# Kernel tuning notes

Measured on AMD Instinct MI355X. Metric: run time of the kernel, lower is better.

## Reference

```python
import jax, jax.numpy as jnp
import numpy as np

B, N, D = 4, 8192, 1024
H, DK = 8, 128          # d_k = D // H
FF = 4096
EPS = 1e-5


def setup_inputs() -> dict:
    key = jax.random.key(0)
    ks = jax.random.split(key, 8)
    s = 0.02  # init scale for weights
    return {
        "x": jax.random.normal(ks[0], (B, N, D), jnp.float32),
        "delta_x": jax.random.uniform(ks[1], (N,), jnp.float32),
        # Linear weights stored [in, out] (math-equivalent to torch's x @ W.T)
        "Wq": jax.random.normal(ks[2], (D, D), jnp.float32) * s,
        "bq": jnp.zeros((D,), jnp.float32),
        "Wk": jax.random.normal(ks[3], (D, D), jnp.float32) * s,
        "bk": jnp.zeros((D,), jnp.float32),
        "Wv": jax.random.normal(ks[4], (D, D), jnp.float32) * s,
        "bv": jnp.zeros((D,), jnp.float32),
        # per-head LayerNorm params for K; NOTE: the original code (faithfully
        # reproduced) applies layernorms_K to BOTH key and value in Galerkin mode.
        "gamma_k": jnp.ones((H, DK), jnp.float32),
        "beta_k": jnp.zeros((H, DK), jnp.float32),
        "W1": jax.random.normal(ks[5], (D, FF), jnp.float32) * s,
        "b1": jnp.zeros((FF,), jnp.float32),
        "W2": jax.random.normal(ks[6], (FF, D), jnp.float32) * s,
        "b2": jnp.zeros((D,), jnp.float32),
    }


def _per_head_ln(t, gamma, beta):
    # t: [B, H, N, DK]; torch LayerNorm: biased variance over last dim
    mu = jnp.mean(t, axis=-1, keepdims=True)
    var = jnp.mean(jnp.square(t - mu), axis=-1, keepdims=True)
    t = (t - mu) * jax.lax.rsqrt(var + EPS)
    return t * gamma[None, :, None, :] + beta[None, :, None, :]


def reference(x, delta_x, Wq, bq, Wk, bk, Wv, bv, gamma_k, beta_k, W1, b1, W2, b2):
    b, n, d = x.shape

    def heads(y):  # [b, n, d] -> [b, H, n, DK]
        return y.reshape(b, n, H, DK).transpose(0, 2, 1, 3)

    q = heads(x @ Wq + bq)
    k = heads(x @ Wk + bk)
    v = heads(x @ Wv + bv)

    k = _per_head_ln(k, gamma_k, beta_k)
    v = _per_head_ln(v, gamma_k, beta_k)  # layernorms_K reused on value (as in source)
    k = k * delta_x[None, None, :, None]  # einsum('bhxd,x->bhxd')

    # Galerkin (softmax-free, linear) attention: (K^T V) / N then Q @ (.)
    scores = jnp.einsum("bhnd,bhne->bhde", k, v) / n  # [b,H,DK,DK]
    attn_out = jnp.einsum("bhnd,bhde->bhne", q, scores)  # [b,H,n,DK]
    # (F.dropout in the source treated as identity: inference/eval semantics)

    x = x + attn_out.transpose(0, 2, 1, 3).reshape(b, n, d)  # residual 1
    h = jax.nn.silu(x @ W1 + b1)
    return x + (h @ W2 + b2)  # residual 2
```

## Files before the change

### kernel.cpp

```cpp
#include <hip/hip_runtime.h>
#include <hip/hip_bf16.h>
#include <stdint.h>

#define DEV __device__ __forceinline__

typedef __attribute__((ext_vector_type(8))) short bf16x8;
typedef __attribute__((ext_vector_type(8))) unsigned short u16x8;
typedef __attribute__((ext_vector_type(4))) unsigned short u16x4;
typedef __attribute__((ext_vector_type(4))) float f32x4;

static constexpr int BB = 4, NN = 8192, DD = 1024, HH = 8, DKK = 128, FFF = 4096;
static constexpr int MM = BB * NN;

DEV float bfb2f(unsigned int s) { unsigned int x = s << 16; float f; __builtin_memcpy(&f, &x, 4); return f; }
DEV unsigned short f2bfb(float f) {
    unsigned int x; __builtin_memcpy(&x, &f, 4);
    x += 0x7fffu + ((x >> 16) & 1u);
    return (unsigned short)(x >> 16);
}

DEV void gload_lds16(const void* g, void* l) {
    auto gp = (const __attribute__((address_space(1))) void*)(uintptr_t)g;
    auto lp = (__attribute__((address_space(3))) void*)(unsigned int)(uintptr_t)l;
    __builtin_amdgcn_global_load_lds(gp, lp, 16, 0, 0);
}

__global__ void k_pack_bf16(const float* __restrict__ in, unsigned short* __restrict__ ob, long n) {
    long i = ((long)blockIdx.x * blockDim.x + threadIdx.x) * 8;
    if (i >= n) return;
    f32x4 a = *(const f32x4*)&in[i];
    f32x4 b = *(const f32x4*)&in[i + 4];
    u16x8 o;
    o[0]=f2bfb(a[0]); o[1]=f2bfb(a[1]); o[2]=f2bfb(a[2]); o[3]=f2bfb(a[3]);
    o[4]=f2bfb(b[0]); o[5]=f2bfb(b[1]); o[6]=f2bfb(b[2]); o[7]=f2bfb(b[3]);
    *(u16x8*)&ob[i] = o;
}

__global__ void k_transpose(const float* __restrict__ W, unsigned short* __restrict__ WT, int R, int C) {
    __shared__ float t[32][33];
    const int tid = threadIdx.x;
    const int r0 = blockIdx.y * 32, c0 = blockIdx.x * 32;
    const int lr = tid >> 3, lc = (tid & 7) * 4;
    f32x4 v = *(const f32x4*)&W[(long)(r0 + lr) * C + c0 + lc];
    t[lr][lc + 0] = v[0]; t[lr][lc + 1] = v[1]; t[lr][lc + 2] = v[2]; t[lr][lc + 3] = v[3];
    __syncthreads();
    const int oc = tid >> 3, orr = (tid & 7) * 4;
    u16x4 o;
    o[0] = f2bfb(t[orr + 0][oc]); o[1] = f2bfb(t[orr + 1][oc]);
    o[2] = f2bfb(t[orr + 2][oc]); o[3] = f2bfb(t[orr + 3][oc]);
    *(u16x4*)&WT[(long)(c0 + oc) * R + r0 + orr] = o;
}

template <int EPI>
__global__ __launch_bounds__(512, 2)
void k_gemm256(const unsigned short* __restrict__ A, int lda,
               const unsigned short* __restrict__ BT, int ldbt,
               const float* __restrict__ bias0, const float* __restrict__ bias1,
               const float* __restrict__ bias2,
               const unsigned short* __restrict__ resb,
               unsigned short* __restrict__ outp0, unsigned short* __restrict__ outp1,
               unsigned short* __restrict__ outp2,
               float* __restrict__ outf,
               int K, int gridx, int npass)
{
    extern __shared__ __align__(128) unsigned short smem[];
    unsigned short* As = smem;
    unsigned short* Bs = smem + 4 * 8192;

    const int wg0 = (blockIdx.x & 7) * 32 + (blockIdx.x >> 3);

    const int tid = threadIdx.x;
    const int lane = tid & 63;
    const int w = tid >> 6;
    const int wm = w >> 2, wn = w & 3;
    const int fr = lane & 15;
    const int kg = lane >> 4;

    const int dl = tid * 16;
    const int soff = dl ^ (((dl >> 7) & 3) << 4);
    const int arow = soff >> 6;
    const int akel = (soff & 63) >> 1;

    int aoff[8], boff[4];
    #pragma unroll
    for (int m = 0; m < 8; ++m) { int o = (wm * 128 + m * 16 + fr) * 64 + kg * 16; aoff[m] = o ^ (((o >> 7) & 3) << 4); }
    #pragma unroll
    for (int n = 0; n < 4; ++n) { int o = (wn * 64 + n * 16 + fr) * 64 + kg * 16; boff[n] = o ^ (((o >> 7) & 3) << 4); }

#define STG_A(base, u, ks, slot) do { \
        const unsigned short* _g = (base) + (long)(u) * 64 + (ks) * 32; \
        gload_lds16(_g,              (slot) + tid * 8); \
        gload_lds16(_g + 128L * lda, (slot) + 4096 + tid * 8); } while (0)
#define STG_B(base, u, ks, slot) do { \
        const unsigned short* _g = (base) + (long)(u) * 64 + (ks) * 32; \
        gload_lds16(_g,               (slot) + tid * 8); \
        gload_lds16(_g + 128L * ldbt, (slot) + 4096 + tid * 8); } while (0)

#define BAR() __builtin_amdgcn_s_barrier()
#define LGKM(N) do { asm volatile("s_waitcnt lgkmcnt(" #N ")" ::: "memory"); \
                     __builtin_amdgcn_sched_barrier(0); } while (0)
#define VM8() asm volatile("s_waitcnt vmcnt(8)" ::: "memory")

#define MFMA16(AF, BF, R0) do { \
        __builtin_amdgcn_s_setprio(1); \
        _Pragma("unroll") \
        for (int m = 0; m < 4; ++m) { \
            _Pragma("unroll") \
            for (int n = 0; n < 4; ++n) \
                acc[(R0) + m][n] = __builtin_amdgcn_mfma_f32_16x16x32_bf16(AF[m], BF[n], acc[(R0) + m][n], 0, 0, 0); \
        } \
        __builtin_amdgcn_s_setprio(0); } while (0)

#define DO_TILE(sa0, sa1, sb0, sb1, STG0, STG1, STG2, STG3) do { \
        bf16x8 b0f[4], a0f[4], a1f[4], b1f[4], a2f[4], a3f[4]; \
        _Pragma("unroll") \
        for (int n = 0; n < 4; ++n) b0f[n] = *(const bf16x8*)((const char*)(sb0) + boff[n]); \
        _Pragma("unroll") \
        for (int m = 0; m < 4; ++m) a0f[m] = *(const bf16x8*)((const char*)(sa0) + aoff[m]); \
        _Pragma("unroll") \
        for (int m = 0; m < 4; ++m) a1f[m] = *(const bf16x8*)((const char*)(sa0) + aoff[m + 4]); \
        STG0; \
        BAR(); LGKM(4); \
        MFMA16(a0f, b0f, 0); \
        BAR(); \
        STG1; VM8(); \
        BAR(); LGKM(0); \
        MFMA16(a1f, b0f, 4); \
        BAR(); \
        _Pragma("unroll") \
        for (int n = 0; n < 4; ++n) b1f[n] = *(const bf16x8*)((const char*)(sb1) + boff[n]); \
        _Pragma("unroll") \
        for (int m = 0; m < 4; ++m) a2f[m] = *(const bf16x8*)((const char*)(sa1) + aoff[m]); \
        _Pragma("unroll") \
        for (int m = 0; m < 4; ++m) a3f[m] = *(const bf16x8*)((const char*)(sa1) + aoff[m + 4]); \
        STG2; \
        BAR(); LGKM(4); \
        MFMA16(a2f, b1f, 0); \
        BAR(); \
        STG3; VM8(); \
        BAR(); LGKM(0); \
        MFMA16(a3f, b1f, 4); \
        BAR(); \
    } while (0)

    unsigned short* A0 = As;            unsigned short* A1 = As + 8192;
    unsigned short* A2 = As + 16384;    unsigned short* A3 = As + 24576;
    unsigned short* B0 = Bs;            unsigned short* B1 = Bs + 8192;
    unsigned short* B2 = Bs + 16384;    unsigned short* B3 = Bs + 24576;

    const int NT = K >> 6;

    int wg = wg0;
    int brow = (wg / gridx) * 256;
    int bcol = (wg % gridx) * 256;
    const unsigned short* Ab = A + (long)(brow + arow) * lda + akel;
    const unsigned short* Bb = BT + (long)(bcol + arow) * ldbt + akel;
    STG_A(Ab, 0, 0, A0); STG_B(Bb, 0, 0, B0);
    STG_B(Bb, 0, 1, B1); STG_A(Ab, 0, 1, A1);
    STG_A(Ab, 1, 0, A2); STG_B(Bb, 1, 0, B2);
    VM8();
    BAR();

    for (int p = 0; p < npass; ++p) {
        const int wgN = (p + 1 < npass) ? (wg0 + (p + 1) * 256) : wg0;
        const int browN = (wgN / gridx) * 256;
        const int bcolN = (wgN % gridx) * 256;
        const unsigned short* Ab2 = A + (long)(browN + arow) * lda + akel;
        const unsigned short* Bb2 = BT + (long)(bcolN + arow) * ldbt + akel;

        f32x4 acc[8][4] = {};

        for (int t = 0; t + 2 < NT; t += 2) {
            DO_TILE(A0, A1, B0, B1,
                    STG_B(Bb, t + 1, 1, B3), STG_A(Ab, t + 1, 1, A3),
                    STG_A(Ab, t + 2, 0, A0), STG_B(Bb, t + 2, 0, B0));
            DO_TILE(A2, A3, B2, B3,
                    STG_B(Bb, t + 2, 1, B1), STG_A(Ab, t + 2, 1, A1),
                    STG_A(Ab, t + 3, 0, A2), STG_B(Bb, t + 3, 0, B2));
        }
        DO_TILE(A0, A1, B0, B1,
                STG_B(Bb, NT - 1, 1, B3), STG_A(Ab, NT - 1, 1, A3),
                STG_A(Ab2, 0, 0, A0), STG_B(Bb2, 0, 0, B0));
        DO_TILE(A2, A3, B2, B3,
                STG_B(Bb2, 0, 1, B1), STG_A(Ab2, 0, 1, A1),
                STG_A(Ab2, 1, 0, A2), STG_B(Bb2, 1, 0, B2));

        const int q4 = (lane >> 4) * 4;
        if constexpr (EPI == 1) {
            const int mat = bcol >> 10;
            const float* bp = mat == 0 ? bias0 : (mat == 1 ? bias1 : bias2);
            unsigned short* op = mat == 0 ? outp0 : (mat == 1 ? outp1 : outp2);
            const int dc0 = bcol & 1023;
            #pragma unroll
            for (int m = 0; m < 8; ++m)
                #pragma unroll
                for (int n = 0; n < 4; ++n) {
                    const int c = dc0 + wn * 64 + n * 16 + fr;
                    const float bv = bp[c];
                    const int hh = c >> 7, dk = c & 127;
                    #pragma unroll
                    for (int j = 0; j < 4; ++j) {
                        const int r = brow + wm * 128 + m * 16 + q4 + j;
                        const long idx = (((long)(r >> 13) * 8 + hh) * 8192 + (r & 8191)) * 128 + dk;
                        op[idx] = f2bfb(acc[m][n][j] + bv);
                    }
                }
        } else if constexpr (EPI == 2) {
            #pragma unroll
            for (int m = 0; m < 8; ++m)
                #pragma unroll
                for (int n = 0; n < 4; ++n) {
                    const int c = bcol + wn * 64 + n * 16 + fr;
                    const float bv = bias0[c];
                    #pragma unroll
                    for (int j = 0; j < 4; ++j) {
                        const int r = brow + wm * 128 + m * 16 + q4 + j;
                        float v = acc[m][n][j] + bv;
                        v = v / (1.f + __expf(-v));
                        outp0[(long)r * FFF + c] = f2bfb(v);
                    }
                }
        } else {
            #pragma unroll
            for (int m = 0; m < 8; ++m)
                #pragma unroll
                for (int n = 0; n < 4; ++n) {
                    const int c = bcol + wn * 64 + n * 16 + fr;
                    const float bv = bias0[c];
                    #pragma unroll
                    for (int j = 0; j < 4; ++j) {
                        const int r = brow + wm * 128 + m * 16 + q4 + j;
                        float v = acc[m][n][j] + bv + bfb2f(resb[(long)r * DD + c]);
                        outf[(long)r * DD + c] = v;
                    }
                }
        }

        brow = browN; bcol = bcolN; Ab = Ab2; Bb = Bb2;
    }
    asm volatile("s_waitcnt vmcnt(0)" ::: "memory");
#undef DO_TILE
#undef MFMA16
#undef VM8
#undef LGKM
#undef BAR
#undef STG_A
#undef STG_B
}

template <int EPI>
__global__ __launch_bounds__(256, 2)
void k_gemm(const unsigned short* __restrict__ A, int lda, long sAz,
            const unsigned short* __restrict__ BT, int ldbt, long sBz,
            const float* __restrict__ bias,
            const float* __restrict__ resf,
            const unsigned short* __restrict__ resb,
            unsigned short* __restrict__ outp,
            float* __restrict__ outf,
            int K)
{
    __shared__ __align__(16) unsigned short As[128 * 32];
    __shared__ __align__(16) unsigned short Bs[128 * 32];
    const int tid = threadIdx.x;
    const int z = blockIdx.z;
    A  += (long)z * sAz;
    BT += (long)z * sBz;
    const int brow = blockIdx.y * 128;
    const int bcol = blockIdx.x * 128;

    const int c0 = tid, c1 = tid + 256;
    const unsigned short* Ap0 = A + (long)(brow + (c0 >> 2)) * lda + (c0 & 3) * 8;
    const unsigned short* Ap1 = A + (long)(brow + (c1 >> 2)) * lda + (c1 & 3) * 8;
    const unsigned short* Bp0 = BT + (long)(bcol + (c0 >> 2)) * ldbt + (c0 & 3) * 8;
    const unsigned short* Bp1 = BT + (long)(bcol + (c1 >> 2)) * ldbt + (c1 & 3) * 8;
    unsigned short* AsD0 = &As[c0 * 8];
    unsigned short* AsD1 = &As[c1 * 8];
    unsigned short* BsD0 = &Bs[c0 * 8];
    unsigned short* BsD1 = &Bs[c1 * 8];

    const int lane = tid & 63;
    const int w = tid >> 6;
    const int wr = (w >> 1) * 64;
    const int wc = (w & 1) * 64;
    const int fr = lane & 15;
    const int fk = (lane >> 4) * 8;

    f32x4 acc[4][4] = {};

    for (int kt = 0; kt < K; kt += 32) {
        gload_lds16(Ap0 + kt, AsD0);
        gload_lds16(Ap1 + kt, AsD1);
        gload_lds16(Bp0 + kt, BsD0);
        gload_lds16(Bp1 + kt, BsD1);
        __syncthreads();
        bf16x8 af[4], bfr[4];
        #pragma unroll
        for (int m = 0; m < 4; ++m) af[m] = *(const bf16x8*)&As[(wr + m * 16 + fr) * 32 + fk];
        #pragma unroll
        for (int n = 0; n < 4; ++n) bfr[n] = *(const bf16x8*)&Bs[(wc + n * 16 + fr) * 32 + fk];
        #pragma unroll
        for (int m = 0; m < 4; ++m)
            #pragma unroll
            for (int n = 0; n < 4; ++n)
                acc[m][n] = __builtin_amdgcn_mfma_f32_16x16x32_bf16(af[m], bfr[n], acc[m][n], 0, 0, 0);
        __syncthreads();
    }

    const int orow = (lane >> 4) * 4;
    #pragma unroll
    for (int m = 0; m < 4; ++m) {
        #pragma unroll
        for (int n = 0; n < 4; ++n) {
            const int d = bcol + wc + n * 16 + fr;
            #pragma unroll
            for (int j = 0; j < 4; ++j) {
                const int r = brow + wr + m * 16 + orow + j;
                float v = acc[m][n][j];
                if constexpr (EPI == 3) {
                    long xi = ((long)(z >> 3) * NN + r) * DD + (z & 7) * DKK + d;
                    v += resf[xi];
                    outp[xi] = f2bfb(v);
                }
            }
        }
    }
    (void)bias; (void)resb; (void)outf;
}

__global__ void k_ln(unsigned short* __restrict__ Kb, unsigned short* __restrict__ Vb,
                     const float* __restrict__ gk, const float* __restrict__ bek,
                     const float* __restrict__ dx)
{
    const int tid = threadIdx.x;
    const int lane = tid & 63;
    const long row = (long)blockIdx.x * 4 + (tid >> 6);
    unsigned short* buf = blockIdx.y ? Vb : Kb;
    const int h = (int)((row >> 13) & 7);
    const int n = (int)(row & 8191);
    unsigned int* p = (unsigned int*)(buf + row * 128) + lane;
    const unsigned int u = *p;
    float f0 = bfb2f(u & 0xffffu);
    float f1 = bfb2f(u >> 16);
    float s = f0 + f1, q = f0 * f0 + f1 * f1;
    #pragma unroll
    for (int o = 32; o; o >>= 1) { s += __shfl_xor(s, o); q += __shfl_xor(q, o); }
    const float mean = s * (1.f / 128.f);
    const float var  = q * (1.f / 128.f) - mean * mean;
    const float rstd = rsqrtf(var + 1e-5f);
    const int gi = h * 128 + lane * 2;
    float o0 = (f0 - mean) * rstd * gk[gi]     + bek[gi];
    float o1 = (f1 - mean) * rstd * gk[gi + 1] + bek[gi + 1];
    if (blockIdx.y == 0) { const float dl = dx[n]; o0 *= dl; o1 *= dl; }
    *p = (unsigned int)f2bfb(o0) | ((unsigned int)f2bfb(o1) << 16);
}

__global__ __launch_bounds__(256, 2)
void k_scorespart(const unsigned short* __restrict__ Kb, const unsigned short* __restrict__ Vb,
                  float* __restrict__ part)
{
    __shared__ __align__(16) unsigned short KT[128 * 136];
    __shared__ __align__(16) unsigned short VT[128 * 136];
    const int tid = threadIdx.x;
    const int bh = blockIdx.y, split = blockIdx.x;
    const unsigned short* Kp = Kb + (long)bh * NN * DKK;
    const unsigned short* Vp = Vb + (long)bh * NN * DKK;
    const int lane = tid & 63, w = tid >> 6;
    const int wr = (w >> 1) * 64, wc = (w & 1) * 64, fr = lane & 15, fk = (lane >> 4) * 8;
    const int nrow = tid >> 1, dblk = (tid & 1) * 64;
    f32x4 acc[4][4] = {};
    for (int c = 0; c < 8; ++c) {
        const int n0 = (split * 8 + c) * 128;
        bf16x8 kv[8], vv[8];
        #pragma unroll
        for (int i = 0; i < 8; ++i) {
            kv[i] = *(const bf16x8*)&Kp[(long)(n0 + nrow) * DKK + dblk + i * 8];
            vv[i] = *(const bf16x8*)&Vp[(long)(n0 + nrow) * DKK + dblk + i * 8];
        }
        __syncthreads();
        #pragma unroll
        for (int i = 0; i < 8; ++i)
            #pragma unroll
            for (int j = 0; j < 8; ++j) {
                const int dd = dblk + i * 8 + j;
                KT[dd * 136 + nrow] = (unsigned short)kv[i][j];
                VT[dd * 136 + nrow] = (unsigned short)vv[i][j];
            }
        __syncthreads();
        #pragma unroll
        for (int ks = 0; ks < 4; ++ks) {
            bf16x8 af[4], bfr[4];
            #pragma unroll
            for (int m = 0; m < 4; ++m) af[m] = *(const bf16x8*)&KT[(wr + m * 16 + fr) * 136 + ks * 32 + fk];
            #pragma unroll
            for (int n = 0; n < 4; ++n) bfr[n] = *(const bf16x8*)&VT[(wc + n * 16 + fr) * 136 + ks * 32 + fk];
            #pragma unroll
            for (int m = 0; m < 4; ++m)
                #pragma unroll
                for (int n = 0; n < 4; ++n)
                    acc[m][n] = __builtin_amdgcn_mfma_f32_16x16x32_bf16(af[m], bfr[n], acc[m][n], 0, 0, 0);
        }
    }
    float* P = part + (long)(bh * 8 + split) * 16384;
    const int orow = (lane >> 4) * 4;
    #pragma unroll
    for (int m = 0; m < 4; ++m)
        #pragma unroll
        for (int n = 0; n < 4; ++n)
            #pragma unroll
            for (int j = 0; j < 4; ++j) {
                const int dD = wr + m * 16 + orow + j;
                const int e  = wc + n * 16 + fr;
                P[dD * 128 + e] = acc[m][n][j];
            }
}

__global__ void k_scoresred(const float* __restrict__ part, unsigned short* __restrict__ scT)
{
    const int bh = blockIdx.x, tid = threadIdx.x;
    const float* P = part + (long)bh * 8 * 16384;
    for (int i = tid; i < 16384; i += 256) {
        float s = 0.f;
        #pragma unroll
        for (int sp = 0; sp < 8; ++sp) s += P[sp * 16384 + i];
        const int d = i >> 7, e = i & 127;
        scT[(long)bh * 16384 + e * 128 + d] = f2bfb(s * (1.f / 8192.f));
    }
}

extern "C" void kernel_launch(void* const* d_in, const int* in_sizes, int n_in,
                              void* d_out, int out_size, void* d_ws, size_t ws_size,
                              hipStream_t stream)
{
    const float* x   = (const float*)d_in[0];
    const float* dx  = (const float*)d_in[1];
    const float* Wq  = (const float*)d_in[2];
    const float* bq  = (const float*)d_in[3];
    const float* Wk  = (const float*)d_in[4];
    const float* bk  = (const float*)d_in[5];
    const float* Wv  = (const float*)d_in[6];
    const float* bv  = (const float*)d_in[7];
    const float* gk  = (const float*)d_in[8];
    const float* bek = (const float*)d_in[9];
    const float* W1  = (const float*)d_in[10];
    const float* b1  = (const float*)d_in[11];
    const float* W2  = (const float*)d_in[12];
    const float* b2  = (const float*)d_in[13];
    float* out = (float*)d_out;
    (void)in_sizes; (void)n_in; (void)out_size; (void)ws_size;

    hipFuncSetAttribute((const void*)k_gemm256<1>, hipFuncAttributeMaxDynamicSharedMemorySize, 131072);
    hipFuncSetAttribute((const void*)k_gemm256<2>, hipFuncAttributeMaxDynamicSharedMemorySize, 131072);
    hipFuncSetAttribute((const void*)k_gemm256<3>, hipFuncAttributeMaxDynamicSharedMemorySize, 131072);

    char* ws = (char*)d_ws;
    size_t off = 0;
    auto alloc = [&](size_t bytes) { void* p = ws + off; off += (bytes + 255) & ~(size_t)255; return p; };
    unsigned short* WqkvT = (unsigned short*)alloc((size_t)3 * DD * DD * 2);
    unsigned short* W1T   = (unsigned short*)alloc((size_t)FFF * DD * 2);
    unsigned short* W2T   = (unsigned short*)alloc((size_t)DD * FFF * 2);
    unsigned short* scT   = (unsigned short*)alloc((size_t)32 * 16384 * 2);
    unsigned short* xb    = (unsigned short*)alloc((size_t)MM * DD * 2);
    unsigned short* Kb    = (unsigned short*)alloc((size_t)MM * DD * 2);
    unsigned short* Vb    = (unsigned short*)alloc((size_t)MM * DD * 2);
    unsigned short* x1b   = (unsigned short*)alloc((size_t)MM * DD * 2);
    unsigned short* hb    = xb;
    float* part           = (float*)x1b;
    unsigned short* Qb    = (unsigned short*)out;

    k_pack_bf16<<<dim3(((long)MM * DD) / 8 / 256), 256, 0, stream>>>(x, xb, (long)MM * DD);
    k_transpose<<<dim3(DD / 32, DD / 32), 256, 0, stream>>>(Wq, WqkvT, DD, DD);
    k_transpose<<<dim3(DD / 32, DD / 32), 256, 0, stream>>>(Wk, WqkvT + (size_t)DD * DD, DD, DD);
    k_transpose<<<dim3(DD / 32, DD / 32), 256, 0, stream>>>(Wv, WqkvT + (size_t)2 * DD * DD, DD, DD);
    k_transpose<<<dim3(FFF / 32, DD / 32), 256, 0, stream>>>(W1, W1T, DD, FFF);
    k_transpose<<<dim3(DD / 32, FFF / 32), 256, 0, stream>>>(W2, W2T, FFF, DD);

    k_gemm256<1><<<dim3(256), 512, 131072, stream>>>(
        xb, DD, WqkvT, DD, bq, bk, bv, nullptr, Qb, Kb, Vb, nullptr, DD, 3072 / 256, 6);

    k_ln<<<dim3((BB * HH * NN) / 4, 2), 256, 0, stream>>>(Kb, Vb, gk, bek, dx);

    k_scorespart<<<dim3(8, 32), 256, 0, stream>>>(Kb, Vb, part);
    k_scoresred<<<dim3(32), 256, 0, stream>>>(part, scT);

    k_gemm<3><<<dim3(1, NN / 128, BB * HH), 256, 0, stream>>>(Qb, DKK, (long)NN * DKK, scT, DKK, 16384L,
                                                              nullptr, x, nullptr, x1b, nullptr, DKK);

    for (int c = 0; c < 2; ++c) {
        const unsigned short* xc = x1b + (size_t)c * 16384 * DD;
        k_gemm256<2><<<dim3(256), 512, 131072, stream>>>(
            xc, DD, W1T, DD, b1, nullptr, nullptr, nullptr, hb, nullptr, nullptr, nullptr, DD, FFF / 256, 4);
        k_gemm256<3><<<dim3(256), 512, 131072, stream>>>(
            hb, FFF, W2T, FFF, b2, nullptr, nullptr, xc, nullptr, nullptr, nullptr,
            out + (size_t)c * 16384 * DD, FFF, DD / 256, 1);
    }
}
```

Baseline: 1.000 ms.

## Fuse per-head LayerNorm and delta scaling into QKV GEMM epilogue

Removes the separate LayerNorm kernel and instead computes per-row mean and variance for K and V heads in the QKV GEMM epilogue. Partial sums are reduced with cross-lane shuffles plus an LDS exchange between the two warps covering each head, which raises dynamic shared memory and adds barriers. It also merges the three QKV weight transposes into one launch, reads the residual from the bf16 copy of x instead of fp32, and reorders the LDS fragment loads in the GEMM main loop so every wait is a full lgkmcnt(0). These cut a full read-and-write pass over K and V and some launch overhead, at the cost of residual precision and possibly less load/compute overlap in the main GEMM loop.

```diff
diff --git a/kernel.cpp b/kernel.cpp
--- a/kernel.cpp
+++ b/kernel.cpp
@@ -36,10 +36,10 @@
     *(u16x8*)&ob[i] = o;
 }
 
-__global__ void k_transpose(const float* __restrict__ W, unsigned short* __restrict__ WT, int R, int C) {
+DEV void transpose_body(const float* __restrict__ W, unsigned short* __restrict__ WT, int R, int C,
+                        int bx, int by, int tid) {
     __shared__ float t[32][33];
-    const int tid = threadIdx.x;
-    const int r0 = blockIdx.y * 32, c0 = blockIdx.x * 32;
+    const int r0 = by * 32, c0 = bx * 32;
     const int lr = tid >> 3, lc = (tid & 7) * 4;
     f32x4 v = *(const f32x4*)&W[(long)(r0 + lr) * C + c0 + lc];
     t[lr][lc + 0] = v[0]; t[lr][lc + 1] = v[1]; t[lr][lc + 2] = v[2]; t[lr][lc + 3] = v[3];
@@ -49,6 +49,14 @@
     o[0] = f2bfb(t[orr + 0][oc]); o[1] = f2bfb(t[orr + 1][oc]);
     o[2] = f2bfb(t[orr + 2][oc]); o[3] = f2bfb(t[orr + 3][oc]);
     *(u16x4*)&WT[(long)(c0 + oc) * R + r0 + orr] = o;
+}
+__global__ void k_transpose(const float* __restrict__ W, unsigned short* __restrict__ WT, int R, int C) {
+    transpose_body(W, WT, R, C, blockIdx.x, blockIdx.y, threadIdx.x);
+}
+__global__ void k_transpose_qkv(const float* __restrict__ Wq, const float* __restrict__ Wk,
+                                const float* __restrict__ Wv, unsigned short* __restrict__ WT) {
+    const float* W = blockIdx.z == 0 ? Wq : (blockIdx.z == 1 ? Wk : Wv);
+    transpose_body(W, WT + (size_t)blockIdx.z * DD * DD, DD, DD, blockIdx.x, blockIdx.y, threadIdx.x);
 }
 
 template <int EPI>
@@ -61,6 +69,8 @@
                unsigned short* __restrict__ outp0, unsigned short* __restrict__ outp1,
                unsigned short* __restrict__ outp2,
                float* __restrict__ outf,
+               const float* __restrict__ gkp, const float* __restrict__ bekp,
+               const float* __restrict__ dxp,
                int K, int gridx, int npass)
 {
     extern __shared__ __align__(128) unsigned short smem[];
@@ -97,7 +107,7 @@
         gload_lds16(_g + 128L * ldbt, (slot) + 4096 + tid * 8); } while (0)
 
 #define BAR() __builtin_amdgcn_s_barrier()
-#define LGKM(N) do { asm volatile("s_waitcnt lgkmcnt(" #N ")" ::: "memory"); \
+#define LGKM0() do { asm volatile("s_waitcnt lgkmcnt(0)" ::: "memory"); \
                      __builtin_amdgcn_sched_barrier(0); } while (0)
 #define VM8() asm volatile("s_waitcnt vmcnt(8)" ::: "memory")
 
@@ -113,32 +123,36 @@
 
 #define DO_TILE(sa0, sa1, sb0, sb1, STG0, STG1, STG2, STG3) do { \
         bf16x8 b0f[4], a0f[4], a1f[4], b1f[4], a2f[4], a3f[4]; \
+         \
         _Pragma("unroll") \
         for (int n = 0; n < 4; ++n) b0f[n] = *(const bf16x8*)((const char*)(sb0) + boff[n]); \
         _Pragma("unroll") \
         for (int m = 0; m < 4; ++m) a0f[m] = *(const bf16x8*)((const char*)(sa0) + aoff[m]); \
-        _Pragma("unroll") \
-        for (int m = 0; m < 4; ++m) a1f[m] = *(const bf16x8*)((const char*)(sa0) + aoff[m + 4]); \
         STG0; \
-        BAR(); LGKM(4); \
+        BAR(); LGKM0(); \
         MFMA16(a0f, b0f, 0); \
         BAR(); \
+         \
+        _Pragma("unroll") \
+        for (int m = 0; m < 4; ++m) a1f[m] = *(const bf16x8*)((const char*)(sa0) + aoff[m + 4]); \
         STG1; VM8(); \
-        BAR(); LGKM(0); \
+        BAR(); LGKM0(); \
         MFMA16(a1f, b0f, 4); \
         BAR(); \
+         \
         _Pragma("unroll") \
         for (int n = 0; n < 4; ++n) b1f[n] = *(const bf16x8*)((const char*)(sb1) + boff[n]); \
         _Pragma("unroll") \
         for (int m = 0; m < 4; ++m) a2f[m] = *(const bf16x8*)((const char*)(sa1) + aoff[m]); \
-        _Pragma("unroll") \
-        for (int m = 0; m < 4; ++m) a3f[m] = *(const bf16x8*)((const char*)(sa1) + aoff[m + 4]); \
         STG2; \
-        BAR(); LGKM(4); \
+        BAR(); LGKM0(); \
         MFMA16(a2f, b1f, 0); \
         BAR(); \
+         \
+        _Pragma("unroll") \
+        for (int m = 0; m < 4; ++m) a3f[m] = *(const bf16x8*)((const char*)(sa1) + aoff[m + 4]); \
         STG3; VM8(); \
-        BAR(); LGKM(0); \
+        BAR(); LGKM0(); \
         MFMA16(a3f, b1f, 4); \
         BAR(); \
     } while (0)
@@ -150,9 +164,8 @@
 
     const int NT = K >> 6;
 
-    int wg = wg0;
-    int brow = (wg / gridx) * 256;
-    int bcol = (wg % gridx) * 256;
+    int brow = ((wg0) / gridx) * 256;
+    int bcol = ((wg0) % gridx) * 256;
     const unsigned short* Ab = A + (long)(brow + arow) * lda + akel;
     const unsigned short* Bb = BT + (long)(bcol + arow) * ldbt + akel;
     STG_A(Ab, 0, 0, A0); STG_B(Bb, 0, 0, B0);
@@ -188,23 +201,87 @@
         const int q4 = (lane >> 4) * 4;
         if constexpr (EPI == 1) {
             const int mat = bcol >> 10;
+            const int dc0 = bcol & 1023;
             const float* bp = mat == 0 ? bias0 : (mat == 1 ? bias1 : bias2);
             unsigned short* op = mat == 0 ? outp0 : (mat == 1 ? outp1 : outp2);
-            const int dc0 = bcol & 1023;
+            float bv[4];
+            #pragma unroll
+            for (int n = 0; n < 4; ++n) bv[n] = bp[dc0 + wn * 64 + n * 16 + fr];
             #pragma unroll
             for (int m = 0; m < 8; ++m)
+                #pragma unroll
+                for (int n = 0; n < 4; ++n)
+                    #pragma unroll
+                    for (int j = 0; j < 4; ++j) acc[m][n][j] += bv[n];
+
+            if (mat == 0) {
+                #pragma unroll
+                for (int m = 0; m < 8; ++m)
+                    #pragma unroll
+                    for (int n = 0; n < 4; ++n) {
+                        const int c = dc0 + wn * 64 + n * 16 + fr;
+                        const int hh = c >> 7, dk = c & 127;
+                        #pragma unroll
+                        for (int j = 0; j < 4; ++j) {
+                            const int r = brow + wm * 128 + m * 16 + q4 + j;
+                            const long idx = (((long)(r >> 13) * 8 + hh) * 8192 + (r & 8191)) * 128 + dk;
+                            op[idx] = f2bfb(acc[m][n][j]);
+                        }
+                    }
+            } else {
+                float2* red2 = (float2*)(smem + 65536);
+                float ps[8][4], pq[8][4];
+                #pragma unroll
+                for (int m = 0; m < 8; ++m)
+                    #pragma unroll
+                    for (int j = 0; j < 4; ++j) {
+                        float s = acc[m][0][j] + acc[m][1][j] + acc[m][2][j] + acc[m][3][j];
+                        float qv = acc[m][0][j] * acc[m][0][j] + acc[m][1][j] * acc[m][1][j]
+                                 + acc[m][2][j] * acc[m][2][j] + acc[m][3][j] * acc[m][3][j];
+                        #pragma unroll
+                        for (int o = 1; o < 16; o <<= 1) { s += __shfl_xor(s, o); qv += __shfl_xor(qv, o); }
+                        ps[m][j] = s; pq[m][j] = qv;
+                    }
+                if (fr == 0) {
+                    const int g4 = lane >> 4;
+                    #pragma unroll
+                    for (int m = 0; m < 8; ++m)
+                        #pragma unroll
+                        for (int j = 0; j < 4; ++j)
+                            red2[wn * 256 + wm * 128 + m * 16 + g4 * 4 + j] = float2{ps[m][j], pq[m][j]};
+                }
+                BAR();
+                float gkv[4], bkv[4];
                 #pragma unroll
                 for (int n = 0; n < 4; ++n) {
                     const int c = dc0 + wn * 64 + n * 16 + fr;
-                    const float bv = bp[c];
-                    const int hh = c >> 7, dk = c & 127;
+                    gkv[n] = gkp[c]; bkv[n] = bekp[c];
+                }
+                const int hbase = (wn >> 1) * 512;
+                #pragma unroll
+                for (int m = 0; m < 8; ++m)
                     #pragma unroll
                     for (int j = 0; j < 4; ++j) {
-                        const int r = brow + wm * 128 + m * 16 + q4 + j;
-                        const long idx = (((long)(r >> 13) * 8 + hh) * 8192 + (r & 8191)) * 128 + dk;
-                        op[idx] = f2bfb(acc[m][n][j] + bv);
+                        const int ri = wm * 128 + m * 16 + q4 + j;
+                        const int r = brow + ri;
+                        const float2 e0 = red2[hbase + ri];
+                        const float2 e1 = red2[hbase + 256 + ri];
+                        const float mean = (e0.x + e1.x) * (1.f / 128.f);
+                        const float var  = (e0.y + e1.y) * (1.f / 128.f) - mean * mean;
+                        const float rstd = rsqrtf(var + 1e-5f);
+                        const float dmul = (mat == 1) ? dxp[r & 8191] : 1.f;
+                        #pragma unroll
+                        for (int n = 0; n < 4; ++n) {
+                            const int c = dc0 + wn * 64 + n * 16 + fr;
+                            const int hh = c >> 7, dk = c & 127;
+                            float v = (acc[m][n][j] - mean) * rstd * gkv[n] + bkv[n];
+                            v *= dmul;
+                            const long idx = (((long)(r >> 13) * 8 + hh) * 8192 + (r & 8191)) * 128 + dk;
+                            op[idx] = f2bfb(v);
+                        }
                     }
-                }
+                BAR();
+            }
         } else if constexpr (EPI == 2) {
             #pragma unroll
             for (int m = 0; m < 8; ++m)
@@ -242,7 +319,7 @@
 #undef DO_TILE
 #undef MFMA16
 #undef VM8
-#undef LGKM
+#undef LGKM0
 #undef BAR
 #undef STG_A
 #undef STG_B
@@ -252,11 +329,8 @@
 __global__ __launch_bounds__(256, 2)
 void k_gemm(const unsigned short* __restrict__ A, int lda, long sAz,
             const unsigned short* __restrict__ BT, int ldbt, long sBz,
-            const float* __restrict__ bias,
-            const float* __restrict__ resf,
             const unsigned short* __restrict__ resb,
             unsigned short* __restrict__ outp,
-            float* __restrict__ outf,
             int K)
 {
     __shared__ __align__(16) unsigned short As[128 * 32];
@@ -315,43 +389,14 @@
             #pragma unroll
             for (int j = 0; j < 4; ++j) {
                 const int r = brow + wr + m * 16 + orow + j;
-                float v = acc[m][n][j];
                 if constexpr (EPI == 3) {
                     long xi = ((long)(z >> 3) * NN + r) * DD + (z & 7) * DKK + d;
-                    v += resf[xi];
+                    float v = acc[m][n][j] + bfb2f(resb[xi]);
                     outp[xi] = f2bfb(v);
                 }
             }
         }
     }
-    (void)bias; (void)resb; (void)outf;
-}
-
-__global__ void k_ln(unsigned short* __restrict__ Kb, unsigned short* __restrict__ Vb,
-                     const float* __restrict__ gk, const float* __restrict__ bek,
-                     const float* __restrict__ dx)
-{
-    const int tid = threadIdx.x;
-    const int lane = tid & 63;
-    const long row = (long)blockIdx.x * 4 + (tid >> 6);
-    unsigned short* buf = blockIdx.y ? Vb : Kb;
-    const int h = (int)((row >> 13) & 7);
-    const int n = (int)(row & 8191);
-    unsigned int* p = (unsigned int*)(buf + row * 128) + lane;
-    const unsigned int u = *p;
-    float f0 = bfb2f(u & 0xffffu);
-    float f1 = bfb2f(u >> 16);
-    float s = f0 + f1, q = f0 * f0 + f1 * f1;
-    #pragma unroll
-    for (int o = 32; o; o >>= 1) { s += __shfl_xor(s, o); q += __shfl_xor(q, o); }
-    const float mean = s * (1.f / 128.f);
-    const float var  = q * (1.f / 128.f) - mean * mean;
-    const float rstd = rsqrtf(var + 1e-5f);
-    const int gi = h * 128 + lane * 2;
-    float o0 = (f0 - mean) * rstd * gk[gi]     + bek[gi];
-    float o1 = (f1 - mean) * rstd * gk[gi + 1] + bek[gi + 1];
-    if (blockIdx.y == 0) { const float dl = dx[n]; o0 *= dl; o1 *= dl; }
-    *p = (unsigned int)f2bfb(o0) | ((unsigned int)f2bfb(o1) << 16);
 }
 
 __global__ __launch_bounds__(256, 2)
@@ -448,7 +493,7 @@
     float* out = (float*)d_out;
     (void)in_sizes; (void)n_in; (void)out_size; (void)ws_size;
 
-    hipFuncSetAttribute((const void*)k_gemm256<1>, hipFuncAttributeMaxDynamicSharedMemorySize, 131072);
+    hipFuncSetAttribute((const void*)k_gemm256<1>, hipFuncAttributeMaxDynamicSharedMemorySize, 139264);
     hipFuncSetAttribute((const void*)k_gemm256<2>, hipFuncAttributeMaxDynamicSharedMemorySize, 131072);
     hipFuncSetAttribute((const void*)k_gemm256<3>, hipFuncAttributeMaxDynamicSharedMemorySize, 131072);
 
@@ -468,29 +513,27 @@
     unsigned short* Qb    = (unsigned short*)out;
 
     k_pack_bf16<<<dim3(((long)MM * DD) / 8 / 256), 256, 0, stream>>>(x, xb, (long)MM * DD);
-    k_transpose<<<dim3(DD / 32, DD / 32), 256, 0, stream>>>(Wq, WqkvT, DD, DD);
-    k_transpose<<<dim3(DD / 32, DD / 32), 256, 0, stream>>>(Wk, WqkvT + (size_t)DD * DD, DD, DD);
-    k_transpose<<<dim3(DD / 32, DD / 32), 256, 0, stream>>>(Wv, WqkvT + (size_t)2 * DD * DD, DD, DD);
+    k_transpose_qkv<<<dim3(DD / 32, DD / 32, 3), 256, 0, stream>>>(Wq, Wk, Wv, WqkvT);
     k_transpose<<<dim3(FFF / 32, DD / 32), 256, 0, stream>>>(W1, W1T, DD, FFF);
     k_transpose<<<dim3(DD / 32, FFF / 32), 256, 0, stream>>>(W2, W2T, FFF, DD);
 
-    k_gemm256<1><<<dim3(256), 512, 131072, stream>>>(
-        xb, DD, WqkvT, DD, bq, bk, bv, nullptr, Qb, Kb, Vb, nullptr, DD, 3072 / 256, 6);
-
-    k_ln<<<dim3((BB * HH * NN) / 4, 2), 256, 0, stream>>>(Kb, Vb, gk, bek, dx);
+    k_gemm256<1><<<dim3(256), 512, 139264, stream>>>(
+        xb, DD, WqkvT, DD, bq, bk, bv, nullptr, Qb, Kb, Vb, nullptr,
+        gk, bek, dx, DD, 3072 / 256, 6);
 
     k_scorespart<<<dim3(8, 32), 256, 0, stream>>>(Kb, Vb, part);
     k_scoresred<<<dim3(32), 256, 0, stream>>>(part, scT);
 
     k_gemm<3><<<dim3(1, NN / 128, BB * HH), 256, 0, stream>>>(Qb, DKK, (long)NN * DKK, scT, DKK, 16384L,
-                                                              nullptr, x, nullptr, x1b, nullptr, DKK);
+                                                              xb, x1b, DKK);
 
     for (int c = 0; c < 2; ++c) {
         const unsigned short* xc = x1b + (size_t)c * 16384 * DD;
         k_gemm256<2><<<dim3(256), 512, 131072, stream>>>(
-            xc, DD, W1T, DD, b1, nullptr, nullptr, nullptr, hb, nullptr, nullptr, nullptr, DD, FFF / 256, 4);
+            xc, DD, W1T, DD, b1, nullptr, nullptr, nullptr, hb, nullptr, nullptr, nullptr,
+            nullptr, nullptr, nullptr, DD, FFF / 256, 4);
         k_gemm256<3><<<dim3(256), 512, 131072, stream>>>(
             hb, FFF, W2T, FFF, b2, nullptr, nullptr, xc, nullptr, nullptr, nullptr,
-            out + (size_t)c * 16384 * DD, FFF, DD / 256, 1);
+            out + (size_t)c * 16384 * DD, nullptr, nullptr, nullptr, FFF, DD / 256, 1);
     }
 }
```

New measurement: 1.073 ms. +7.2%, slower.
